# Performance work log

Measured on AMD Instinct MI355X. Metric: run time of the kernel, lower is better.

## Reference

```python
import jax, jax.numpy as jnp
import numpy as np

NUM_GROUPS = 8   # num_groups1, recursive_index=False path
NUM_HEADS = 8


def setup_inputs() -> dict:
    key = jax.random.key(0)
    k1, k2, k3 = jax.random.split(key, 3)
    B, C, H, W = 4, 256, 64, 64
    x = jax.random.normal(k1, (B, C, H, W), dtype=jnp.float32)
    w_qkv = jax.random.normal(k2, (3 * C, C), dtype=jnp.float32) * 0.02
    w_proj = jax.random.normal(k3, (C, C), dtype=jnp.float32) * 0.02
    b_proj = jnp.zeros((C,), dtype=jnp.float32)
    return {"x": x, "w_qkv": w_qkv, "w_proj": w_proj, "b_proj": b_proj}


def reference(x, w_qkv, w_proj, b_proj):
    B, C, H, W = x.shape
    N = H * W
    G = NUM_GROUPS
    nh = NUM_HEADS
    hd = C // nh
    M = N // G
    scale = hd ** -0.5

    # b c h w -> b (h w) c
    xf = x.reshape(B, C, N).transpose(0, 2, 1)  # [B, N, C]

    # qkv linear (no bias), then split into groups / heads
    qkv = (xf @ w_qkv.T).reshape(B, G, M, 3, nh, hd)
    qkv = jnp.transpose(qkv, (3, 0, 1, 4, 2, 5))  # [3, B, G, nh, M, hd]
    q, k, v = qkv[0], qkv[1], qkv[2]

    # grouped multi-head attention, manual softmax
    attn = jax.nn.softmax(jnp.einsum('bghmd,bghnd->bghmn', q, k) * scale, axis=-1)
    out = jnp.einsum('bghmn,bghnd->bghmd', attn, v)

    # [B,G,nh,M,hd] -> [B,G,M,C] -> [B,N,C]
    out = out.transpose(0, 1, 3, 2, 4).reshape(B, N, C)

    out = out @ w_proj.T + b_proj

    # b (h w) c -> b c h w
    return out.transpose(0, 2, 1).reshape(B, C, H, W)
```

## Files before the change

### kernel.cpp

```cpp
#include <hip/hip_runtime.h>
#include <hip/hip_bf16.h>

#define Bb 4
#define Cc 256
#define Nn 4096
#define Gg 8
#define NHh 8
#define HDd 32
#define Mm 512

typedef __bf16 bf16_t;
typedef __bf16 bf16x2 __attribute__((ext_vector_type(2)));
typedef __bf16 bf16x4 __attribute__((ext_vector_type(4)));
typedef __bf16 bf16x8 __attribute__((ext_vector_type(8)));
typedef float f32x4 __attribute__((ext_vector_type(4)));

#define LSCALE (0.17677669529663687f * 1.44269504088896340f)

__device__ __forceinline__ void load_lds16(const bf16_t* g, bf16_t* l) {
  __builtin_amdgcn_global_load_lds(
      (const __attribute__((address_space(1))) void*)g,
      (__attribute__((address_space(3))) void*)l, 16, 0, 0);
}

__global__ __launch_bounds__(256) void prep_kernel(
    const float* __restrict__ x, bf16_t* __restrict__ xT,
    const float* __restrict__ wqkv, const float* __restrict__ wproj,
    bf16_t* __restrict__ wq_b, bf16_t* __restrict__ wp_b) {
  int bid = blockIdx.x, tid = threadIdx.x;
  if (bid >= 1024) {
    int i = (bid - 1024) * 256 + tid;
    wq_b[i] = (bf16_t)wqkv[i];
    if (i < Cc * Cc) wp_b[i] = (bf16_t)wproj[i];
    return;
  }
  __shared__ float t[64][65];
  int b = bid >> 8, c0 = ((bid >> 6) & 3) * 64, n0 = (bid & 63) * 64;
  const float* xp = x + ((long long)b * Cc + c0) * Nn + n0;
#pragma unroll
  for (int it = 0; it < 4; ++it) {
    int idx = it * 256 + tid;
    int r = idx >> 4, col = (idx & 15) * 4;
    f32x4 v = *(const f32x4*)&xp[(long long)r * Nn + col];
    t[r][col] = v[0];
    t[r][col + 1] = v[1];
    t[r][col + 2] = v[2];
    t[r][col + 3] = v[3];
  }
  __syncthreads();
  bf16_t* op = xT + ((long long)b * Nn + n0) * Cc + c0;
#pragma unroll
  for (int it = 0; it < 2; ++it) {
    int idx = it * 256 + tid;
    int n = idx >> 3, cg = (idx & 7) * 8;
    bf16x8 w;
#pragma unroll
    for (int j = 0; j < 8; ++j) w[j] = (bf16_t)t[cg + j][n];
    *(bf16x8*)&op[(long long)n * Cc + cg] = w;
  }
}

__global__ __launch_bounds__(256, 4) void qkv_gemm_kernel(
    const bf16_t* __restrict__ xT, const bf16_t* __restrict__ wqb,
    bf16_t* __restrict__ Qh, bf16_t* __restrict__ Kh, bf16_t* __restrict__ Vh) {
  __shared__ bf16_t smem[20480];
  int pb = blockIdx.x;
  int bid = (pb & 7) * 96 + (pb >> 3);
  int m0 = (bid / 3) * 64;
  int n0 = (bid % 3) * 256;
  int tid = threadIdx.x, lane = tid & 63, wid = tid >> 6;
  int quad = lane >> 4, l16 = lane & 15;
  int wn = wid * 64;

  f32x4 acc[4][4];
#pragma unroll
  for (int i = 0; i < 4; ++i)
#pragma unroll
    for (int j = 0; j < 4; ++j) acc[i][j] = (f32x4){0.f, 0.f, 0.f, 0.f};

  int scol = (lane & 3) * 8;
  int arow = lane >> 2;
  auto stage = [&](int bufi, int k0) {
    load_lds16(&xT[(long long)(m0 + wid * 16 + arow) * Cc + k0 + scol],
               &smem[bufi * 2048 + wid * 512]);
#pragma unroll
    for (int r = 0; r < 4; ++r) {
      int ch = wid * 4 + r;
      load_lds16(&wqb[(long long)(n0 + ch * 16 + arow) * Cc + k0 + scol],
                 &smem[4096 + bufi * 8192 + ch * 512]);
    }
  };

  stage(0, 0);
  __syncthreads();
  for (int t = 0; t < 8; ++t) {
    if (t < 7) stage((t + 1) & 1, (t + 1) * 32);
    const bf16_t* Ap = &smem[(t & 1) * 2048];
    const bf16_t* Bp = &smem[4096 + (t & 1) * 8192];
    bf16x8 a[4], b[4];
#pragma unroll
    for (int i = 0; i < 4; ++i)
      a[i] = *(const bf16x8*)&Ap[(i * 16 + l16) * 32 + quad * 8];
#pragma unroll
    for (int j = 0; j < 4; ++j)
      b[j] = *(const bf16x8*)&Bp[(wn + j * 16 + l16) * 32 + quad * 8];
#pragma unroll
    for (int i = 0; i < 4; ++i)
#pragma unroll
      for (int j = 0; j < 4; ++j)
        acc[i][j] = __builtin_amdgcn_mfma_f32_16x16x32_bf16(a[i], b[j], acc[i][j], 0, 0, 0);
    __syncthreads();
  }

  if (n0 < 512) {
    const bool isQ = (n0 == 0);
    const float s = isQ ? LSCALE : 1.0f;
#pragma unroll
    for (int i = 0; i < 4; ++i)
#pragma unroll
      for (int j = 0; j < 4; ++j) {
        int f = wn + j * 16 + l16;
#pragma unroll
        for (int r = 0; r < 4; ++r) {
          int lm = i * 16 + quad * 4 + r;
          smem[lm * 268 + f] = (bf16_t)(acc[i][j][r] * s);
        }
      }
    __syncthreads();
    int lm = tid >> 2, d0 = (tid & 3) * 8;
    int row = m0 + lm;
    int bb = row >> 12, gg = (row >> 9) & 7, m = row & 511;
    bf16_t* dst = isQ ? Qh : Kh;
#pragma unroll
    for (int hh = 0; hh < 8; ++hh) {
      long long hb = (long long)((bb << 6) | (gg << 3) | hh) * (Mm * HDd);
      bf16x8 w = *(bf16x8*)&smem[lm * 268 + hh * 32 + d0];
      *(bf16x8*)&dst[hb + m * HDd + d0] = w;
    }
  } else {
#pragma unroll
    for (int i = 0; i < 4; ++i)
#pragma unroll
      for (int j = 0; j < 4; ++j) {
        int f = wn + j * 16 + l16;
#pragma unroll
        for (int r = 0; r < 4; ++r)
          smem[f * 72 + i * 16 + quad * 4 + r] = (bf16_t)acc[i][j][r];
      }
    __syncthreads();
    int bb = m0 >> 12, gg = (m0 >> 9) & 7, mb = m0 & 511;
#pragma unroll
    for (int it = 0; it < 8; ++it) {
      int idx = it * 256 + tid;
      int f = idx >> 3, seg = idx & 7;
      int hh = f >> 5, d = f & 31;
      long long hb = (long long)((bb << 6) | (gg << 3) | hh) * (Mm * HDd);
      bf16x8 w = *(bf16x8*)&smem[f * 72 + seg * 8];
      *(bf16x8*)&Vh[hb + (long long)d * Mm + mb + seg * 8] = w;
    }
  }
}

__global__ __launch_bounds__(256, 4) void attn_kernel(
    const bf16_t* __restrict__ Qh, const bf16_t* __restrict__ Kh,
    const bf16_t* __restrict__ Vh, bf16_t* __restrict__ Oa) {
  __shared__ bf16_t Ks[256 * 32];
  __shared__ bf16_t Vs[32 * 264];
  int pg = blockIdx.x;
  int gid = (pg & 7) * 128 + (pg >> 3);
  int ms = gid & 3, head = gid >> 2;
  int h = head & 7, g = (head >> 3) & 7, b = head >> 6;
  int tid = threadIdx.x, lane = tid & 63, wid = tid >> 6;
  int quad = lane >> 4, l16 = lane & 15;

  const bf16_t* Kg = Kh + (long long)head * (Mm * HDd);
  const bf16_t* Vg = Vh + (long long)head * (Mm * HDd);
  const bf16_t* Qg = Qh + (long long)head * (Mm * HDd) + (ms * 128 + wid * 32) * HDd;

  bf16x8 qa = *(const bf16x8*)&Qg[l16 * HDd + quad * 8];
  bf16x8 qb = *(const bf16x8*)&Qg[(16 + l16) * HDd + quad * 8];

  bf16x8 ones;
#pragma unroll
  for (int i = 0; i < 8; ++i) ones[i] = (bf16_t)1.0f;

  int rp0 = ((l16 >> 2) << 3) | (l16 & 3);
  const bf16_t* Kp0 = &Ks[rp0 * HDd + quad * 8];
  const bf16_t* Kp1 = Kp0 + 4 * HDd;
  const bf16_t* VsL = &Vs[l16 * 264 + quad * 8];
  const bf16_t* VsH = &Vs[(16 + l16) * 264 + quad * 8];
  const f32x4 zero = (f32x4){0.f, 0.f, 0.f, 0.f};

  f32x4 oLa = zero, oHa = zero, oLb = zero, oHb = zero;
  f32x4 ra = zero, rb = zero;

  auto inner = [&]() {
#pragma unroll
    for (int c = 0; c < 8; ++c) {
      int nb = c * 32;
      bf16x8 kf0 = *(const bf16x8*)&Kp0[nb * HDd];
      bf16x8 kf1 = *(const bf16x8*)&Kp1[nb * HDd];
      f32x4 sa0 = __builtin_amdgcn_mfma_f32_16x16x32_bf16(kf0, qa, zero, 0, 0, 0);
      f32x4 sa1 = __builtin_amdgcn_mfma_f32_16x16x32_bf16(kf1, qa, zero, 0, 0, 0);
      f32x4 sb0 = __builtin_amdgcn_mfma_f32_16x16x32_bf16(kf0, qb, zero, 0, 0, 0);
      f32x4 sb1 = __builtin_amdgcn_mfma_f32_16x16x32_bf16(kf1, qb, zero, 0, 0, 0);
      bf16x8 pa, pb;
#pragma unroll
      for (int r = 0; r < 4; ++r) {
        pa[r] = (bf16_t)__builtin_exp2f(sa0[r]);
        pa[4 + r] = (bf16_t)__builtin_exp2f(sa1[r]);
        pb[r] = (bf16_t)__builtin_exp2f(sb0[r]);
        pb[4 + r] = (bf16_t)__builtin_exp2f(sb1[r]);
      }
      bf16x8 vL = *(const bf16x8*)&VsL[nb];
      bf16x8 vH = *(const bf16x8*)&VsH[nb];
      oLa = __builtin_amdgcn_mfma_f32_16x16x32_bf16(vL, pa, oLa, 0, 0, 0);
      oHa = __builtin_amdgcn_mfma_f32_16x16x32_bf16(vH, pa, oHa, 0, 0, 0);
      oLb = __builtin_amdgcn_mfma_f32_16x16x32_bf16(vL, pb, oLb, 0, 0, 0);
      oHb = __builtin_amdgcn_mfma_f32_16x16x32_bf16(vH, pb, oHb, 0, 0, 0);
      ra = __builtin_amdgcn_mfma_f32_16x16x32_bf16(ones, pa, ra, 0, 0, 0);
      rb = __builtin_amdgcn_mfma_f32_16x16x32_bf16(ones, pb, rb, 0, 0, 0);
    }
  };

#pragma unroll
  for (int it = 0; it < 4; ++it) {
    int ch = wid * 4 + it;
    load_lds16(&Kg[ch * 512 + lane * 8], &Ks[ch * 512]);
  }
  bf16x8 vcur[4], vnxt[4];
#pragma unroll
  for (int i = 0; i < 4; ++i) {
    int idx = i * 256 + tid;
    int d = idx >> 5, c16 = idx & 31;
    vcur[i] = *(const bf16x8*)&Vg[d * Mm + c16 * 8];
    vnxt[i] = *(const bf16x8*)&Vg[d * Mm + 256 + c16 * 8];
  }
#pragma unroll
  for (int i = 0; i < 4; ++i) {
    int idx = i * 256 + tid;
    int d = idx >> 5, c16 = idx & 31;
    *(bf16x8*)&Vs[d * 264 + c16 * 8] = vcur[i];
  }
  __syncthreads();
  inner();
  __syncthreads();
#pragma unroll
  for (int it = 0; it < 4; ++it) {
    int ch = wid * 4 + it;
    load_lds16(&Kg[8192 + ch * 512 + lane * 8], &Ks[ch * 512]);
  }
#pragma unroll
  for (int i = 0; i < 4; ++i) {
    int idx = i * 256 + tid;
    int d = idx >> 5, c16 = idx & 31;
    *(bf16x8*)&Vs[d * 264 + c16 * 8] = vnxt[i];
  }
  __syncthreads();
  inner();

  float inva = 1.f / ra[0], invb = 1.f / rb[0];

  long long orowa =
      ((long long)(b * Nn + g * Mm + ms * 128 + wid * 32 + l16)) * Cc + h * HDd;
  long long orowb = orowa + 16 * Cc;
  bf16x4 wLa, wHa, wLb, wHb;
#pragma unroll
  for (int r = 0; r < 4; ++r) {
    wLa[r] = (bf16_t)(oLa[r] * inva);
    wHa[r] = (bf16_t)(oHa[r] * inva);
    wLb[r] = (bf16_t)(oLb[r] * invb);
    wHb[r] = (bf16_t)(oHb[r] * invb);
  }
  *(bf16x4*)&Oa[orowa + quad * 4] = wLa;
  *(bf16x4*)&Oa[orowa + 16 + quad * 4] = wHa;
  *(bf16x4*)&Oa[orowb + quad * 4] = wLb;
  *(bf16x4*)&Oa[orowb + 16 + quad * 4] = wHb;
}

__global__ __launch_bounds__(256, 4) void proj_kernel(
    const bf16_t* __restrict__ Wp, const bf16_t* __restrict__ Oa,
    float* __restrict__ out, const float* __restrict__ bias) {
  __shared__ bf16_t As[2][64 * 32];
  __shared__ bf16_t Bs[2][64 * 32];
  int tid = threadIdx.x, lane = tid & 63, wid = tid >> 6;
  int quad = lane >> 4, l16 = lane & 15;
  int z = blockIdx.z;
  const bf16_t* Bt = Oa + (long long)z * Nn * Cc;
  int m0 = blockIdx.y * 64, n0 = blockIdx.x * 64;

  f32x4 acc[4];
#pragma unroll
  for (int i = 0; i < 4; ++i) acc[i] = (f32x4){0.f, 0.f, 0.f, 0.f};

  int scol = (lane & 3) * 8;
  int arow = lane >> 2;
  auto stage = [&](int bufi, int k0) {
    load_lds16(&Wp[(long long)(m0 + wid * 16 + arow) * Cc + k0 + scol],
               &As[bufi][wid * 512]);
    load_lds16(&Bt[(long long)(n0 + wid * 16 + arow) * Cc + k0 + scol],
               &Bs[bufi][wid * 512]);
  };

  stage(0, 0);
  __syncthreads();
  for (int t = 0; t < 8; ++t) {
    if (t < 7) stage((t + 1) & 1, (t + 1) * 32);
    const bf16_t* Ap = As[t & 1];
    const bf16_t* Bp = Bs[t & 1];
    bf16x8 a[4], b;
#pragma unroll
    for (int i = 0; i < 4; ++i)
      a[i] = *(const bf16x8*)&Ap[(i * 16 + l16) * 32 + quad * 8];
    b = *(const bf16x8*)&Bp[(wid * 16 + l16) * 32 + quad * 8];
#pragma unroll
    for (int i = 0; i < 4; ++i)
      acc[i] = __builtin_amdgcn_mfma_f32_16x16x32_bf16(a[i], b, acc[i], 0, 0, 0);
    __syncthreads();
  }

#pragma unroll
  for (int i = 0; i < 4; ++i) {
    int col = n0 + wid * 16 + l16;
#pragma unroll
    for (int r = 0; r < 4; ++r) {
      int row = m0 + i * 16 + quad * 4 + r;
      out[(long long)z * (Cc * Nn) + (long long)row * Nn + col] =
          acc[i][r] + bias[row];
    }
  }
}

extern "C" void kernel_launch(void* const* d_in, const int* in_sizes, int n_in,
                              void* d_out, int out_size, void* d_ws, size_t ws_size,
                              hipStream_t stream) {
  (void)in_sizes; (void)n_in; (void)out_size; (void)ws_size;
  const float* x = (const float*)d_in[0];
  const float* w_qkv = (const float*)d_in[1];
  const float* w_proj = (const float*)d_in[2];
  const float* b_proj = (const float*)d_in[3];
  float* out = (float*)d_out;

  char* ws = (char*)d_ws;
  bf16_t* xT  = (bf16_t*)(ws);
  bf16_t* wqb = (bf16_t*)(ws + 8388608);
  bf16_t* wpb = (bf16_t*)(ws + 8781824);
  bf16_t* Qh  = (bf16_t*)(ws + 8912896);
  bf16_t* Kh  = (bf16_t*)(ws + 17301504);
  bf16_t* Vh  = (bf16_t*)(ws + 25690112);
  bf16_t* Oa  = (bf16_t*)(ws + 34078720);

  prep_kernel<<<1792, 256, 0, stream>>>(x, xT, w_qkv, w_proj, wqb, wpb);
  qkv_gemm_kernel<<<768, 256, 0, stream>>>(xT, wqb, Qh, Kh, Vh);
  attn_kernel<<<1024, 256, 0, stream>>>(Qh, Kh, Vh, Oa);
  proj_kernel<<<dim3(64, 4, 4), 256, 0, stream>>>(wpb, Oa, out, b_proj);
}
```

Measured before the change: 118.6 us.

## Swizzle LDS tile layouts in GEMM and attention kernels to avoid bank conflicts

Applies an XOR swizzle to the 16-byte chunk column when staging A/B tiles into LDS via global_load_lds in the QKV GEMM, projection GEMM and the attention K tile. The fragment reads use the matching swizzled offsets. The aim is to cut LDS bank conflicts on the bf16x8 fragment reads. It also raises wave priority with s_setprio around the attention inner MFMA loop, which adds a little index math and risks a mismatched swizzle if any row mapping is wrong.

```diff
diff --git a/kernel.cpp b/kernel.cpp
--- a/kernel.cpp
+++ b/kernel.cpp
@@ -22,6 +22,7 @@
       (const __attribute__((address_space(1))) void*)g,
       (__attribute__((address_space(3))) void*)l, 16, 0, 0);
 }
+
 
 __global__ __launch_bounds__(256) void prep_kernel(
     const float* __restrict__ x, bf16_t* __restrict__ xT,
@@ -78,18 +79,20 @@
 #pragma unroll
     for (int j = 0; j < 4; ++j) acc[i][j] = (f32x4){0.f, 0.f, 0.f, 0.f};
 
-  int scol = (lane & 3) * 8;
+  int scolz = (((lane & 3) ^ ((lane >> 4) ^ (lane >> 2))) & 3) * 8;
   int arow = lane >> 2;
   auto stage = [&](int bufi, int k0) {
-    load_lds16(&xT[(long long)(m0 + wid * 16 + arow) * Cc + k0 + scol],
+    load_lds16(&xT[(long long)(m0 + wid * 16 + arow) * Cc + k0 + scolz],
                &smem[bufi * 2048 + wid * 512]);
 #pragma unroll
     for (int r = 0; r < 4; ++r) {
       int ch = wid * 4 + r;
-      load_lds16(&wqb[(long long)(n0 + ch * 16 + arow) * Cc + k0 + scol],
+      load_lds16(&wqb[(long long)(n0 + ch * 16 + arow) * Cc + k0 + scolz],
                  &smem[4096 + bufi * 8192 + ch * 512]);
     }
   };
+
+  int qz = ((quad ^ ((l16 >> 2) ^ l16)) & 3) * 8;
 
   stage(0, 0);
   __syncthreads();
@@ -100,10 +103,10 @@
     bf16x8 a[4], b[4];
 #pragma unroll
     for (int i = 0; i < 4; ++i)
-      a[i] = *(const bf16x8*)&Ap[(i * 16 + l16) * 32 + quad * 8];
+      a[i] = *(const bf16x8*)&Ap[(i * 16 + l16) * 32 + qz];
 #pragma unroll
     for (int j = 0; j < 4; ++j)
-      b[j] = *(const bf16x8*)&Bp[(wn + j * 16 + l16) * 32 + quad * 8];
+      b[j] = *(const bf16x8*)&Bp[(wn + j * 16 + l16) * 32 + qz];
 #pragma unroll
     for (int i = 0; i < 4; ++i)
 #pragma unroll
@@ -184,9 +187,12 @@
 #pragma unroll
   for (int i = 0; i < 8; ++i) ones[i] = (bf16_t)1.0f;
 
+  int scolz = (((lane & 3) ^ ((lane >> 4) ^ (lane >> 2))) & 3) * 8;
+
   int rp0 = ((l16 >> 2) << 3) | (l16 & 3);
-  const bf16_t* Kp0 = &Ks[rp0 * HDd + quad * 8];
-  const bf16_t* Kp1 = Kp0 + 4 * HDd;
+  int rkey0 = (((rp0 >> 2) ^ rp0) & 3);
+  const bf16_t* Kp0 = &Ks[rp0 * HDd + ((quad ^ rkey0) & 3) * 8];
+  const bf16_t* Kp1 = &Ks[(rp0 + 4) * HDd + ((quad ^ rkey0 ^ 1) & 3) * 8];
   const bf16_t* VsL = &Vs[l16 * 264 + quad * 8];
   const bf16_t* VsH = &Vs[(16 + l16) * 264 + quad * 8];
   const f32x4 zero = (f32x4){0.f, 0.f, 0.f, 0.f};
@@ -195,6 +201,7 @@
   f32x4 ra = zero, rb = zero;
 
   auto inner = [&]() {
+    __builtin_amdgcn_s_setprio(1);
 #pragma unroll
     for (int c = 0; c < 8; ++c) {
       int nb = c * 32;
@@ -221,12 +228,13 @@
       ra = __builtin_amdgcn_mfma_f32_16x16x32_bf16(ones, pa, ra, 0, 0, 0);
       rb = __builtin_amdgcn_mfma_f32_16x16x32_bf16(ones, pb, rb, 0, 0, 0);
     }
+    __builtin_amdgcn_s_setprio(0);
   };
 
 #pragma unroll
   for (int it = 0; it < 4; ++it) {
     int ch = wid * 4 + it;
-    load_lds16(&Kg[ch * 512 + lane * 8], &Ks[ch * 512]);
+    load_lds16(&Kg[ch * 512 + (lane >> 2) * 32 + scolz], &Ks[ch * 512]);
   }
   bf16x8 vcur[4], vnxt[4];
 #pragma unroll
@@ -248,7 +256,7 @@
 #pragma unroll
   for (int it = 0; it < 4; ++it) {
     int ch = wid * 4 + it;
-    load_lds16(&Kg[8192 + ch * 512 + lane * 8], &Ks[ch * 512]);
+    load_lds16(&Kg[8192 + ch * 512 + (lane >> 2) * 32 + scolz], &Ks[ch * 512]);
   }
 #pragma unroll
   for (int i = 0; i < 4; ++i) {
@@ -293,14 +301,16 @@
 #pragma unroll
   for (int i = 0; i < 4; ++i) acc[i] = (f32x4){0.f, 0.f, 0.f, 0.f};
 
-  int scol = (lane & 3) * 8;
+  int scolz = (((lane & 3) ^ ((lane >> 4) ^ (lane >> 2))) & 3) * 8;
   int arow = lane >> 2;
   auto stage = [&](int bufi, int k0) {
-    load_lds16(&Wp[(long long)(m0 + wid * 16 + arow) * Cc + k0 + scol],
+    load_lds16(&Wp[(long long)(m0 + wid * 16 + arow) * Cc + k0 + scolz],
                &As[bufi][wid * 512]);
-    load_lds16(&Bt[(long long)(n0 + wid * 16 + arow) * Cc + k0 + scol],
+    load_lds16(&Bt[(long long)(n0 + wid * 16 + arow) * Cc + k0 + scolz],
                &Bs[bufi][wid * 512]);
   };
+
+  int qz = ((quad ^ ((l16 >> 2) ^ l16)) & 3) * 8;
 
   stage(0, 0);
   __syncthreads();
@@ -311,8 +321,8 @@
     bf16x8 a[4], b;
 #pragma unroll
     for (int i = 0; i < 4; ++i)
-      a[i] = *(const bf16x8*)&Ap[(i * 16 + l16) * 32 + quad * 8];
-    b = *(const bf16x8*)&Bp[(wid * 16 + l16) * 32 + quad * 8];
+      a[i] = *(const bf16x8*)&Ap[(i * 16 + l16) * 32 + qz];
+    b = *(const bf16x8*)&Bp[(wid * 16 + l16) * 32 + qz];
 #pragma unroll
     for (int i = 0; i < 4; ++i)
       acc[i] = __builtin_amdgcn_mfma_f32_16x16x32_bf16(a[i], b, acc[i], 0, 0, 0);
```

Result: slower. 123.6 us (+4.2%).
